# Performance work log

Measured on AMD Instinct MI355X. Metric: run time of the kernel, lower is better.

The kernel has to match this reference:

```python
import jax, jax.numpy as jnp
import numpy as np

B, N, E, D, F_IN, EDGE_DIM, VN = 128, 500, 1048576, 128, 5, 2, 10
NEG_FEAT = 0.01   # torch F.leaky_relu default
NEG_ATT = 0.2     # GAT attention slope


def _gat_layer(h_in, src, dst, edge_attr, W, b, a_src, a_dst, a_edge, We, n_nodes):
    # Edge-feature GAT conv: per-edge attention over (src, dst, edge) then
    # softmax-normalized scatter-aggregate onto destination nodes.
    h = h_in @ W                                  # [N, d]
    e = edge_attr @ We                            # [E, d] projected edge features
    logits = jax.nn.leaky_relu((h @ a_src)[src] + (h @ a_dst)[dst] + e @ a_edge,
                               negative_slope=NEG_ATT)    # [E]
    # segment softmax over incoming edges of each dst node
    m = jax.ops.segment_max(logits, dst, num_segments=n_nodes)
    ex = jnp.exp(logits - m[dst])
    denom = jax.ops.segment_sum(ex, dst, num_segments=n_nodes)
    alpha = ex / (denom[dst] + 1e-16)             # [E]
    msg = h[src] + e                              # [E, d]
    out = jax.ops.segment_sum(alpha[:, None] * msg, dst, num_segments=n_nodes)
    return out + b


def setup_inputs() -> dict:
    key = jax.random.key(0)
    ks = jax.random.split(key, 20)
    s = 0.05
    return {
        'x': jax.random.normal(ks[0], (B * N, F_IN), jnp.float32),
        'edge_index': jax.random.randint(ks[1], (2, E), 0, B * N, jnp.int64 if jax.config.jax_enable_x64 else jnp.int32).astype(jnp.int32),
        'edge_attr': jax.random.uniform(ks[2], (E, EDGE_DIM), jnp.float32),
        'curr_v_node_id': jax.random.randint(ks[3], (B,), 0, VN).astype(jnp.int32),
        'v_graph_embedding': jax.random.normal(ks[4], (B, D), jnp.float32),
        'v_node_dense_embeddings': jax.random.normal(ks[5], (B, VN, D), jnp.float32),
        'p_W': jax.random.normal(ks[6], (F_IN, D), jnp.float32) * s,
        'p_b': jnp.zeros((D,), jnp.float32),
        'Ws': jax.random.normal(ks[7], (4, D, D), jnp.float32) * s,
        'bs': jnp.zeros((4, D), jnp.float32),
        'a_srcs': jax.random.normal(ks[8], (4, D), jnp.float32) * s,
        'a_dsts': jax.random.normal(ks[9], (4, D), jnp.float32) * s,
        'a_edges': jax.random.normal(ks[10], (4, D), jnp.float32) * s,
        'Wes': jax.random.normal(ks[11], (4, EDGE_DIM, D), jnp.float32) * s,
        'W5': jax.random.normal(ks[12], (D, 1), jnp.float32) * s,
        'b5': jnp.zeros((1,), jnp.float32),
        'a_src5': jax.random.normal(ks[13], (1,), jnp.float32) * s,
        'a_dst5': jax.random.normal(ks[14], (1,), jnp.float32) * s,
        'a_edge5': jax.random.normal(ks[15], (1,), jnp.float32) * s,
        'We5': jax.random.normal(ks[16], (EDGE_DIM, 1), jnp.float32) * s,
    }


def reference(x, edge_index, edge_attr, curr_v_node_id, v_graph_embedding,
              v_node_dense_embeddings, p_W, p_b, Ws, bs, a_srcs, a_dsts,
              a_edges, Wes, W5, b5, a_src5, a_dst5, a_edge5, We5):
    n_nodes = x.shape[0]
    src, dst = edge_index[0], edge_index[1]
    # gather current v-node embedding: [B, D]
    curr_emb = v_node_dense_embeddings[jnp.arange(B), curr_v_node_id]
    # linear + leaky_relu then broadcast-add of graph/node context
    h = jax.nn.leaky_relu(x @ p_W + p_b, negative_slope=NEG_FEAT)  # [B*N, D]
    h = h.reshape(B, N, D) + v_graph_embedding[:, None, :] + curr_emb[:, None, :]
    h = h.reshape(B * N, D)
    # 4 hidden edge-feature GAT layers (128 -> 128) with leaky_relu
    for l in range(4):
        h = _gat_layer(h, src, dst, edge_attr, Ws[l], bs[l], a_srcs[l],
                       a_dsts[l], a_edges[l], Wes[l], n_nodes)
        h = jax.nn.leaky_relu(h, negative_slope=NEG_FEAT)
    # output layer (128 -> 1), no activation
    h = _gat_layer(h, src, dst, edge_attr, W5, b5, a_src5, a_dst5, a_edge5,
                   We5, n_nodes)                    # [B*N, 1]
    return h.reshape(B, N)
```

## Files before the change

kernel.cpp:

```cpp
#include <hip/hip_runtime.h>
#include <hip/hip_bf16.h>

#define BB   128
#define NN   500
#define NV   64000
#define EE   1048576
#define DD   128
#define FIN  5
#define VNN  10
#define NBUK 250
#define BCAP 8192

typedef unsigned int   uint32;
typedef unsigned short u16b;
typedef __attribute__((ext_vector_type(8))) short short8;
typedef __attribute__((ext_vector_type(4))) float float4v;

#define P_ASRC  0
#define P_ADST  512
#define P_WE    1024
#define P_BIAS  2048
#define P_W5    2560
#define P_CVEC  2688
#define P_SC5   2700
#define P_TOT   2816

static __device__ __forceinline__ float bf2f(__hip_bfloat16 v) { return __bfloat162float(v); }
static __device__ __forceinline__ float lo2f(uint32 u) { return __uint_as_float(u << 16); }
static __device__ __forceinline__ float hi2f(uint32 u) { return __uint_as_float(u & 0xFFFF0000u); }
static __device__ __forceinline__ uint32 f2bf_bits(float f) {
    uint32 u = __float_as_uint(f);
    return (u + 0x7FFFu + ((u >> 16) & 1u)) >> 16;
}
static __device__ __forceinline__ uint32 pack2(float a, float b) {
    return (f2bf_bits(a) & 0xFFFFu) | (f2bf_bits(b) << 16);
}
static __device__ __forceinline__ float ldf(const void* p, int i, int flag) {
    return flag ? ((const float*)p)[i] : bf2f(((const __hip_bfloat16*)p)[i]);
}

__global__ void sniff_kernel(const unsigned short* __restrict__ p16, int* __restrict__ FLAG) {
    __shared__ int sHigh, sZero;
    if (threadIdx.x == 0) { sHigh = 0; sZero = 0; }
    __syncthreads();
    unsigned short v = p16[2 * threadIdx.x];
    if (v >= 0x8000u) atomicOr(&sHigh, 1);
    if (v == 0)       atomicAdd(&sZero, 1);
    __syncthreads();
    if (threadIdx.x == 0) FLAG[0] = (sHigh || sZero >= 128) ? 1 : 0;
}

__global__ void zero_out_kernel(void* __restrict__ out, const int* __restrict__ FLAG, float tag) {
    int i = blockIdx.x * blockDim.x + threadIdx.x;
    if (i >= NV) return;
    float v = (i == 0) ? tag : 0.f;
    if (FLAG[0]) ((float*)out)[i] = v;
    else         ((u16b*)out)[i] = (u16b)f2bf_bits(v);
}

__global__ void prep_kernel(const void* __restrict__ Wes, const void* __restrict__ aeg,
                            const void* __restrict__ We5, const void* __restrict__ ae5,
                            const void* __restrict__ asr, const void* __restrict__ ads,
                            const void* __restrict__ bs, const void* __restrict__ W5,
                            const void* __restrict__ b5, const void* __restrict__ as5,
                            const void* __restrict__ ad5, const int* __restrict__ FLAG,
                            float* __restrict__ PAR) {
    const int flag = FLAG[0];
    if (blockIdx.x == 0) {
        for (int i = threadIdx.x; i < 512; i += 256) PAR[P_ASRC + i] = ldf(asr, i, flag);
    } else if (blockIdx.x == 1) {
        for (int i = threadIdx.x; i < 512; i += 256) PAR[P_ADST + i] = ldf(ads, i, flag);
    } else if (blockIdx.x == 2) {
        for (int i = threadIdx.x; i < 1024; i += 256) PAR[P_WE + i] = ldf(Wes, i, flag);
    } else if (blockIdx.x == 3) {
        for (int i = threadIdx.x; i < 512; i += 256) PAR[P_BIAS + i] = ldf(bs, i, flag);
    } else if (blockIdx.x == 4) {
        int tid = threadIdx.x;
        if (tid < 128) {
            PAR[P_W5 + tid] = ldf(W5, tid, flag);
        } else if (tid < 136) {
            int l = (tid - 128) >> 1, r = (tid - 128) & 1;
            float s = 0.f;
            for (int ch = 0; ch < DD; ++ch)
                s += ldf(Wes, l * 256 + r * DD + ch, flag) * ldf(aeg, l * DD + ch, flag);
            PAR[P_CVEC + l * 2 + r] = s;
        } else if (tid == 136) {
            float ae = ldf(ae5, 0, flag);
            float w0 = ldf(We5, 0, flag), w1 = ldf(We5, 1, flag);
            PAR[P_CVEC + 8] = w0 * ae; PAR[P_CVEC + 9] = w1 * ae;
            PAR[P_CVEC + 10] = w0;     PAR[P_CVEC + 11] = w1;
            PAR[P_SC5 + 0] = ldf(b5, 0, flag);
            PAR[P_SC5 + 1] = ldf(as5, 0, flag);
            PAR[P_SC5 + 2] = ldf(ad5, 0, flag);
        }
    }
}

__global__ __launch_bounds__(256) void prepack_kernel(const void* __restrict__ Ws,
                                                      const int* __restrict__ FLAG,
                                                      u16b* __restrict__ WB) {
    const int flag = FLAG[0];
    int t = blockIdx.x * 256 + threadIdx.x;
    int lane = t & 63;
    int frag = t >> 6;
    int nchunk = frag & 7, kblk = (frag >> 3) & 3, l = frag >> 5;
    int n = nchunk * 16 + (lane & 15);
    int kbase = kblk * 32 + (lane >> 4) * 8;
#pragma unroll
    for (int j = 0; j < 8; ++j) {
        int idx = l * 16384 + (kbase + j) * 128 + n;
        u16b bits = flag ? (u16b)f2bf_bits(((const float*)Ws)[idx])
                         : ((const u16b*)Ws)[idx];
        WB[(size_t)t * 8 + j] = bits;
    }
}

__global__ __launch_bounds__(256) void proj_kernel(
        const void* __restrict__ x, const void* __restrict__ pW,
        const void* __restrict__ pb, const int* __restrict__ curr,
        const void* __restrict__ vge, const void* __restrict__ vnd,
        const int* __restrict__ FLAG, uint32* __restrict__ H) {
    const int flag = FLAG[0];
    const int n = blockIdx.x * 4 + (threadIdx.x >> 6);
    const int lane = threadIdx.x & 63;
    const int b = n / NN;
    int cv = curr[b]; if ((unsigned)cv >= VNN) cv = 0;
    float xv[FIN];
#pragma unroll
    for (int k = 0; k < FIN; ++k) xv[k] = ldf(x, n * FIN + k, flag);
    const int ch = lane * 2;
    float s0 = ldf(pb, ch, flag), s1 = ldf(pb, ch + 1, flag);
#pragma unroll
    for (int k = 0; k < FIN; ++k) {
        s0 = fmaf(xv[k], ldf(pW, k * DD + ch, flag), s0);
        s1 = fmaf(xv[k], ldf(pW, k * DD + ch + 1, flag), s1);
    }
    s0 = (s0 > 0.f) ? s0 : 0.01f * s0;
    s1 = (s1 > 0.f) ? s1 : 0.01f * s1;
    s0 += ldf(vge, b * DD + ch, flag) + ldf(vnd, (b * VNN + cv) * DD + ch, flag);
    s1 += ldf(vge, b * DD + ch + 1, flag) + ldf(vnd, (b * VNN + cv) * DD + ch + 1, flag);
    H[(size_t)n * 64 + lane] = pack2(s0, s1);
}

__global__ void init_kernel(int* __restrict__ gcur, int* __restrict__ counts) {
    int t = blockIdx.x * 256 + threadIdx.x;
    if (t < NBUK) gcur[t] = t * BCAP;
    if (t < 512) counts[NV + t] = 0;
}

__global__ __launch_bounds__(256) void bucketize_kernel(
        const int* __restrict__ src, const int* __restrict__ dst,
        const void* __restrict__ eaP, const int* __restrict__ FLAG,
        int* __restrict__ gcur, uint32* __restrict__ bukx, uint32* __restrict__ buky) {
    __shared__ int cnt[256];
    __shared__ int cur[256];
    const int flag = FLAG[0];
    const int t = threadIdx.x;
    const int e0 = blockIdx.x * 4096;
    cnt[t] = 0;
    __syncthreads();
    int d[16];
#pragma unroll
    for (int i = 0; i < 16; ++i) {
        d[i] = dst[e0 + i * 256 + t];
        if ((unsigned)d[i] >= NV) d[i] = -1;
        if (d[i] >= 0) atomicAdd(&cnt[d[i] >> 8], 1);
    }
    __syncthreads();
    if (t < NBUK) {
        int c = cnt[t];
        cur[t] = c ? atomicAdd(&gcur[t], c) : 0;
    }
    __syncthreads();
#pragma unroll
    for (int i = 0; i < 16; ++i) {
        if (d[i] < 0) continue;
        int e = e0 + i * 256 + t;
        int b = d[i] >> 8;
        int s = src[e];
        if ((unsigned)s >= NV) s = 0;
        uint32 eb;
        if (flag) { float2 v = ((const float2*)eaP)[e]; eb = pack2(v.x, v.y); }
        else      eb = ((const uint32*)eaP)[e];
        int p = atomicAdd(&cur[b], 1);
        if (p < (b + 1) * BCAP) {
            bukx[p] = (uint32)((s & 0xFFFF) | ((d[i] & 255) << 16));
            buky[p] = eb;
        }
    }
}

__global__ __launch_bounds__(256) void bcount_kernel(
        const uint32* __restrict__ bukx, const int* __restrict__ gcur,
        int* __restrict__ counts) {
    __shared__ int c[256];
    const int b = blockIdx.x, t = threadIdx.x;
    c[t] = 0;
    __syncthreads();
    const int base = b * BCAP;
    int cnt = gcur[b] - base;
    if (cnt > BCAP) cnt = BCAP;
    for (int i = t; i < cnt; i += 256)
        atomicAdd(&c[(bukx[base + i] >> 16) & 255], 1);
    __syncthreads();
    counts[b * 256 + t] = c[t];
}

__global__ __launch_bounds__(256) void scan1_kernel(const int* __restrict__ counts,
                                                    int* __restrict__ row_ptr,
                                                    int* __restrict__ partials) {
    __shared__ int sdata[256];
    int tid = threadIdx.x;
    int4 v = ((const int4*)counts)[blockIdx.x * 256 + tid];
    int sum = v.x + v.y + v.z + v.w;
    sdata[tid] = sum;
    __syncthreads();
    int acc = sum;
    for (int off = 1; off < 256; off <<= 1) {
        int t = (tid >= off) ? sdata[tid - off] : 0;
        __syncthreads();
        acc += t;
        sdata[tid] = acc;
        __syncthreads();
    }
    int excl = acc - sum;
    int base = blockIdx.x * 1024 + tid * 4;
    int run = excl;
    if (base + 0 <= NV) row_ptr[base + 0] = run; run += v.x;
    if (base + 1 <= NV) row_ptr[base + 1] = run; run += v.y;
    if (base + 2 <= NV) row_ptr[base + 2] = run; run += v.z;
    if (base + 3 <= NV) row_ptr[base + 3] = run;
    if (tid == 255) partials[blockIdx.x] = acc;
}

__global__ __launch_bounds__(64) void scan2_kernel(const int* __restrict__ partials,
                                                   int* __restrict__ boff, int nb) {
    int lane = threadIdx.x;
    int v = (lane < nb) ? partials[lane] : 0;
    int orig = v;
#pragma unroll
    for (int off = 1; off < 64; off <<= 1) {
        int t = __shfl_up(v, off, 64);
        if (lane >= off) v += t;
    }
    boff[lane] = v - orig;
}

__global__ __launch_bounds__(256) void scan3_kernel(int* __restrict__ row_ptr,
                                                    const int* __restrict__ boff) {
    int add = boff[blockIdx.x];
    int base = blockIdx.x * 1024 + threadIdx.x * 4;
#pragma unroll
    for (int j = 0; j < 4; ++j) {
        int i = base + j;
        if (i <= NV) row_ptr[i] += add;
    }
}

__global__ __launch_bounds__(256) void bscatter_kernel(
        const uint32* __restrict__ bukx, const uint32* __restrict__ buky,
        const int* __restrict__ gcur, const int* __restrict__ row_ptr,
        int* __restrict__ csr_src, uint32* __restrict__ csr_ea) {
    __shared__ int cur[256];
    const int b = blockIdx.x, t = threadIdx.x;
    cur[t] = row_ptr[b * 256 + t];
    __syncthreads();
    const int base = b * BCAP;
    int cnt = gcur[b] - base;
    if (cnt > BCAP) cnt = BCAP;
    for (int i = t; i < cnt; i += 256) {
        uint32 x = bukx[base + i];
        uint32 y = buky[base + i];
        int p = atomicAdd(&cur[(x >> 16) & 255], 1);
        csr_src[p] = (int)(x & 0xFFFFu);
        csr_ea[p] = y;
    }
}

__global__ __launch_bounds__(256) void gemm_kernel(
        const uint32* __restrict__ Hu, const u16b* __restrict__ WBl,
        const float* __restrict__ PARl, uint32* __restrict__ HWu,
        float* __restrict__ ssrc, float* __restrict__ sdst) {
    __shared__ float hs[64 * 129];
    __shared__ float pp[512];
    const int tid = threadIdx.x;
    const int lane = tid & 63;
    const int wave = tid >> 6;
    const int quad = lane >> 4;
    const int n0 = blockIdx.x * 64;
    const int m = n0 + wave * 16 + (lane & 15);

    const u16b* hrow = (const u16b*)Hu + (size_t)m * 128;
    short8 a0 = *(const short8*)(hrow + 0  + quad * 8);
    short8 a1 = *(const short8*)(hrow + 32 + quad * 8);
    short8 a2 = *(const short8*)(hrow + 64 + quad * 8);
    short8 a3 = *(const short8*)(hrow + 96 + quad * 8);

#pragma unroll
    for (int nt = 0; nt < 8; ++nt) {
        const u16b* bbase = WBl + ((size_t)nt * 512 + lane * 8);
        short8 b0 = *(const short8*)(bbase + 0 * 4096);
        short8 b1 = *(const short8*)(bbase + 1 * 4096);
        short8 b2 = *(const short8*)(bbase + 2 * 4096);
        short8 b3 = *(const short8*)(bbase + 3 * 4096);
        float4v acc = {0.f, 0.f, 0.f, 0.f};
        acc = __builtin_amdgcn_mfma_f32_16x16x32_bf16(a0, b0, acc, 0, 0, 0);
        acc = __builtin_amdgcn_mfma_f32_16x16x32_bf16(a1, b1, acc, 0, 0, 0);
        acc = __builtin_amdgcn_mfma_f32_16x16x32_bf16(a2, b2, acc, 0, 0, 0);
        acc = __builtin_amdgcn_mfma_f32_16x16x32_bf16(a3, b3, acc, 0, 0, 0);
#pragma unroll
        for (int r = 0; r < 4; ++r)
            hs[(wave * 16 + quad * 4 + r) * 129 + nt * 16 + (lane & 15)] = acc[r];
    }
    __syncthreads();

    {
        const int mn = tid & 63, cg = tid >> 6;
        const float* Asr = PARl + P_ASRC;
        const float* Ads = PARl + P_ADST;
        const float* row = hs + mn * 129 + cg * 32;
        float ps = 0.f, pd = 0.f;
#pragma unroll
        for (int j = 0; j < 32; ++j) {
            float v = row[j];
            ps = fmaf(v, Asr[cg * 32 + j], ps);
            pd = fmaf(v, Ads[cg * 32 + j], pd);
        }
        pp[tid] = ps; pp[256 + tid] = pd;
    }
    __syncthreads();
    if (tid < 64) {
        ssrc[n0 + tid] = pp[tid] + pp[64 + tid] + pp[128 + tid] + pp[192 + tid];
        sdst[n0 + tid] = pp[256 + tid] + pp[320 + tid] + pp[384 + tid] + pp[448 + tid];
    }

#pragma unroll
    for (int i = 0; i < 4; ++i) {
        int flat = i * 2048 + tid * 8;
        int n = flat >> 7, c = flat & 127;
        const float* p = hs + n * 129 + c;
        uint4 v;
        v.x = pack2(p[0], p[1]); v.y = pack2(p[2], p[3]);
        v.z = pack2(p[4], p[5]); v.w = pack2(p[6], p[7]);
        *(uint4*)(HWu + (size_t)(n0 + n) * 64 + c / 2) = v;
    }
}

__global__ __launch_bounds__(256) void agg_kernel(
        const uint32* __restrict__ HWu, const float* __restrict__ ssrc,
        const float* __restrict__ sdst, const int* __restrict__ csr_src,
        const uint32* __restrict__ csr_ea, const int* __restrict__ row_ptr,
        const float* __restrict__ PAR, int layer, uint32* __restrict__ HoutU,
        float* __restrict__ hw5out, int wantw5) {
    const int lane = threadIdx.x & 63;
    const int n = blockIdx.x * 4 + (threadIdx.x >> 6);
    const int begin = __builtin_amdgcn_readfirstlane(row_ptr[n]);
    const int deg   = __builtin_amdgcn_readfirstlane(row_ptr[n + 1]) - begin;
    const float c0 = PAR[P_CVEC + 2 * layer], c1 = PAR[P_CVEC + 2 * layer + 1];
    const float sd = sdst[n];

    int   sv = 0;
    uint32 eb = 0;
    float L = -3.4e38f;
    if (lane < deg) {
        sv = csr_src[begin + lane];
        eb = csr_ea[begin + lane];
        L = fmaf(hi2f(eb), c1, fmaf(lo2f(eb), c0, ssrc[sv] + sd));
        L = (L > 0.f) ? L : 0.2f * L;
    }
    float m = L;
    for (int j0 = 64; j0 < deg; j0 += 64) {
        int j = j0 + lane;
        if (j < deg) {
            int s2 = csr_src[begin + j];
            uint32 e2 = csr_ea[begin + j];
            float L2 = fmaf(hi2f(e2), c1, fmaf(lo2f(e2), c0, ssrc[s2] + sd));
            L2 = (L2 > 0.f) ? L2 : 0.2f * L2;
            m = fmaxf(m, L2);
        }
    }
#pragma unroll
    for (int o = 32; o; o >>= 1) m = fmaxf(m, __shfl_xor(m, o, 64));

    float ex = (lane < deg) ? __expf(L - m) : 0.f;
    float dsum = ex, sx = ex * lo2f(eb), sy = ex * hi2f(eb);
    for (int j0 = 64; j0 < deg; j0 += 64) {
        int j = j0 + lane;
        if (j < deg) {
            int s2 = csr_src[begin + j];
            uint32 e2 = csr_ea[begin + j];
            float L2 = fmaf(hi2f(e2), c1, fmaf(lo2f(e2), c0, ssrc[s2] + sd));
            L2 = (L2 > 0.f) ? L2 : 0.2f * L2;
            float x2 = __expf(L2 - m);
            dsum += x2; sx = fmaf(x2, lo2f(e2), sx); sy = fmaf(x2, hi2f(e2), sy);
        }
    }
#pragma unroll
    for (int o = 32; o; o >>= 1) {
        dsum += __shfl_xor(dsum, o, 64);
        sx   += __shfl_xor(sx, o, 64);
        sy   += __shfl_xor(sy, o, 64);
    }

    const int dmain = (deg < 64) ? deg : 64;
    const uint32 exu = __float_as_uint(ex);
    float acc0 = 0.f, acc1 = 0.f;
    int jj = 0;
    for (; jj + 8 <= dmain; jj += 8) {
        int s8[8]; float e8[8]; uint32 hv[8];
#pragma unroll
        for (int q = 0; q < 8; ++q) {
            s8[q] = __builtin_amdgcn_readlane(sv, jj + q);
            e8[q] = __uint_as_float(__builtin_amdgcn_readlane((int)exu, jj + q));
        }
#pragma unroll
        for (int q = 0; q < 8; ++q) hv[q] = HWu[(size_t)s8[q] * 64 + lane];
#pragma unroll
        for (int q = 0; q < 8; ++q) {
            acc0 = fmaf(e8[q], lo2f(hv[q]), acc0);
            acc1 = fmaf(e8[q], hi2f(hv[q]), acc1);
        }
    }
    for (; jj < dmain; ++jj) {
        int s = __builtin_amdgcn_readlane(sv, jj);
        float e1v = __uint_as_float(__builtin_amdgcn_readlane((int)exu, jj));
        uint32 hb = HWu[(size_t)s * 64 + lane];
        acc0 = fmaf(e1v, lo2f(hb), acc0);
        acc1 = fmaf(e1v, hi2f(hb), acc1);
    }
    for (jj = 64; jj < deg; ++jj) {
        int s = csr_src[begin + jj];
        uint32 e2 = csr_ea[begin + jj];
        float L2 = fmaf(hi2f(e2), c1, fmaf(lo2f(e2), c0, ssrc[s] + sd));
        L2 = (L2 > 0.f) ? L2 : 0.2f * L2;
        float x2 = __expf(L2 - m);
        uint32 hb = HWu[(size_t)s * 64 + lane];
        acc0 = fmaf(x2, lo2f(hb), acc0);
        acc1 = fmaf(x2, hi2f(hb), acc1);
    }

    const int ch = lane * 2;
    const float* WEl = PAR + P_WE + layer * 256;
    const float inv = 1.f / (dsum + 1e-16f);
    const float* Bl = PAR + P_BIAS + layer * DD;
    float t0 = fmaf(sy, WEl[DD + ch],     fmaf(sx, WEl[ch],     acc0));
    float t1 = fmaf(sy, WEl[DD + ch + 1], fmaf(sx, WEl[ch + 1], acc1));
    float o0 = fmaf(t0, inv, Bl[ch]);
    float o1 = fmaf(t1, inv, Bl[ch + 1]);
    o0 = (o0 > 0.f) ? o0 : 0.01f * o0;
    o1 = (o1 > 0.f) ? o1 : 0.01f * o1;
    HoutU[(size_t)n * 64 + lane] = pack2(o0, o1);

    if (wantw5) {
        float p = o0 * PAR[P_W5 + ch] + o1 * PAR[P_W5 + ch + 1];
#pragma unroll
        for (int o = 32; o; o >>= 1) p += __shfl_xor(p, o, 64);
        if (lane == 0) hw5out[n] = p;
    }
}

__global__ __launch_bounds__(256) void final_kernel(
        const float* __restrict__ hw5, const int* __restrict__ csr_src,
        const uint32* __restrict__ csr_ea, const int* __restrict__ row_ptr,
        const float* __restrict__ PAR, const int* __restrict__ FLAG,
        void* __restrict__ out) {
    const int flag = FLAG[0];
    int lane = threadIdx.x & 63;
    int n = blockIdx.x * 4 + (threadIdx.x >> 6);
    int begin = __builtin_amdgcn_readfirstlane(row_ptr[n]);
    int deg   = __builtin_amdgcn_readfirstlane(row_ptr[n + 1]) - begin;
    float c50 = PAR[P_CVEC + 8], c51 = PAR[P_CVEC + 9];
    float ce0 = PAR[P_CVEC + 10], ce1 = PAR[P_CVEC + 11];
    float b5v = PAR[P_SC5], a5s = PAR[P_SC5 + 1];
    float hd = PAR[P_SC5 + 2] * hw5[n];

    float m = -3.4e38f;
    for (int j0 = 0; j0 < deg; j0 += 64) {
        int j = j0 + lane;
        if (j < deg) {
            int s = csr_src[begin + j];
            uint32 eb = csr_ea[begin + j];
            float L = fmaf(hi2f(eb), c51, fmaf(lo2f(eb), c50, fmaf(a5s, hw5[s], hd)));
            L = (L > 0.f) ? L : 0.2f * L;
            m = fmaxf(m, L);
        }
    }
#pragma unroll
    for (int o = 32; o; o >>= 1) m = fmaxf(m, __shfl_xor(m, o, 64));

    float dsum = 0.f, msum = 0.f;
    for (int j0 = 0; j0 < deg; j0 += 64) {
        int j = j0 + lane;
        if (j < deg) {
            int s = csr_src[begin + j];
            uint32 eb = csr_ea[begin + j];
            float hs5 = hw5[s];
            float L = fmaf(hi2f(eb), c51, fmaf(lo2f(eb), c50, fmaf(a5s, hs5, hd)));
            L = (L > 0.f) ? L : 0.2f * L;
            float ex = __expf(L - m);
            dsum += ex;
            msum = fmaf(ex, hs5 + fmaf(hi2f(eb), ce1, lo2f(eb) * ce0), msum);
        }
    }
#pragma unroll
    for (int o = 32; o; o >>= 1) {
        dsum += __shfl_xor(dsum, o, 64);
        msum += __shfl_xor(msum, o, 64);
    }
    if (lane == 0) {
        float r = msum / (dsum + 1e-16f) + b5v;
        if (flag) ((float*)out)[n] = r;
        else      ((u16b*)out)[n] = (u16b)f2bf_bits(r);
    }
}

extern "C" void kernel_launch(void* const* d_in, const int* in_sizes, int n_in,
                              void* d_out, int out_size, void* d_ws, size_t ws_size,
                              hipStream_t stream) {
    const void* x   = d_in[0];
    const int*  ei  = (const int*)d_in[1];
    const void* ea  = d_in[2];
    const int*  cur = (const int*)d_in[3];
    const void* vge = d_in[4];
    const void* vnd = d_in[5];
    const void* pW  = d_in[6];
    const void* pb  = d_in[7];
    const void* Ws  = d_in[8];
    const void* bs  = d_in[9];
    const void* asr = d_in[10];
    const void* ads = d_in[11];
    const void* aeg = d_in[12];
    const void* Wes = d_in[13];
    const void* W5  = d_in[14];
    const void* b5  = d_in[15];
    const void* as5 = d_in[16];
    const void* ad5 = d_in[17];
    const void* ae5 = d_in[18];
    const void* We5 = d_in[19];
    (void)in_sizes; (void)n_in; (void)out_size;

    const int* e_src = ei;
    const int* e_dst = ei + EE;

    size_t off = 0;
    char* base = (char*)d_ws;
    auto carve = [&](size_t bytes) {
        void* p = base + off;
        off += (bytes + 255) & ~(size_t)255;
        return p;
    };
    int*    FLAG   = (int*)carve(256);
    float*  PAR    = (float*)carve((size_t)P_TOT * 4);
    u16b*   WB     = (u16b*)carve(4 * DD * DD * 2);
    uint32* H0     = (uint32*)carve((size_t)NV * DD * 2);
    uint32* H1     = (uint32*)carve((size_t)NV * DD * 2);
    float*  SS     = (float*)carve(NV * 4);
    float*  SD     = (float*)carve(NV * 4);
    float*  HW5v   = (float*)carve(NV * 4);
    int*    COUNTS = (int*)carve(65536 * 4);
    int*    ROWPTR = (int*)carve(65536 * 4);
    int*    GCUR   = (int*)carve(256 * 4);
    int*    PART   = (int*)carve(256 * 4);
    int*    BOFF   = (int*)carve(256 * 4);
    int*    CSRS   = (int*)carve((size_t)EE * 4);
    uint32* CSREA  = (uint32*)carve((size_t)EE * 4);
    size_t need = off;

    uint32* BUKX = H1;
    uint32* BUKY = H1 + (size_t)NBUK * BCAP;

    sniff_kernel<<<1, 256, 0, stream>>>((const unsigned short*)ea, FLAG);

    if (need > ws_size) {
        zero_out_kernel<<<(NV + 255) / 256, 256, 0, stream>>>(
            d_out, FLAG, (float)(ws_size >> 20));
        return;
    }

    prep_kernel<<<5, 256, 0, stream>>>(Wes, aeg, We5, ae5, asr, ads, bs,
                                       W5, b5, as5, ad5, FLAG, PAR);
    prepack_kernel<<<32, 256, 0, stream>>>(Ws, FLAG, WB);
    proj_kernel<<<NV / 4, 256, 0, stream>>>(x, pW, pb, cur, vge, vnd, FLAG, H0);

    init_kernel<<<2, 256, 0, stream>>>(GCUR, COUNTS);
    bucketize_kernel<<<EE / 4096, 256, 0, stream>>>(e_src, e_dst, ea, FLAG,
                                                    GCUR, BUKX, BUKY);
    bcount_kernel<<<NBUK, 256, 0, stream>>>(BUKX, GCUR, COUNTS);
    scan1_kernel<<<63, 256, 0, stream>>>(COUNTS, ROWPTR, PART);
    scan2_kernel<<<1, 64, 0, stream>>>(PART, BOFF, 63);
    scan3_kernel<<<63, 256, 0, stream>>>(ROWPTR, BOFF);
    bscatter_kernel<<<NBUK, 256, 0, stream>>>(BUKX, BUKY, GCUR, ROWPTR,
                                              CSRS, CSREA);

    for (int l = 0; l < 4; ++l) {
        gemm_kernel<<<NV / 64, 256, 0, stream>>>(
            H0, WB + (size_t)l * 16384, PAR + l * DD, H1, SS, SD);
        agg_kernel<<<NV / 4, 256, 0, stream>>>(
            H1, SS, SD, CSRS, CSREA, ROWPTR, PAR, l, H0, HW5v, (l == 3) ? 1 : 0);
    }

    final_kernel<<<NV / 4, 256, 0, stream>>>(HW5v, CSRS, CSREA, ROWPTR, PAR,
                                             FLAG, d_out);
}
```

Before: 467.0 us.

## Prefetch neighbor feature rows before softmax in aggregation kernel

Issues the gathers of neighbour HW rows for the first 16 or 32 edges into registers before the max and softmax reductions, so that memory latency overlaps with the logit and exp computation. The weighted accumulation then reads the prefetched registers, and a scalar loop handles edges 32 to 63. Padded lanes use src index 0 with zero weight, so the extra loads are harmless. The 32 extra registers per thread may lower occupancy.

```diff
diff --git a/kernel.cpp b/kernel.cpp
--- a/kernel.cpp
+++ b/kernel.cpp
@@ -361,11 +361,32 @@
 
     int   sv = 0;
     uint32 eb = 0;
-    float L = -3.4e38f;
     if (lane < deg) {
         sv = csr_src[begin + lane];
         eb = csr_ea[begin + lane];
-        L = fmaf(hi2f(eb), c1, fmaf(lo2f(eb), c0, ssrc[sv] + sd));
+    }
+    const float ssv = ssrc[sv];
+
+    const int dmain = (deg < 64) ? deg : 64;
+    const int npad  = (dmain + 15) & ~15;
+
+    uint32 hA[16], hB[16];
+#pragma unroll
+    for (int q = 0; q < 16; ++q) {
+        int s = __builtin_amdgcn_readlane(sv, q);
+        hA[q] = HWu[(s << 6) + lane];
+    }
+    if (npad > 16) {
+#pragma unroll
+        for (int q = 0; q < 16; ++q) {
+            int s = __builtin_amdgcn_readlane(sv, 16 + q);
+            hB[q] = HWu[(s << 6) + lane];
+        }
+    }
+
+    float L = -3.4e38f;
+    if (lane < deg) {
+        L = fmaf(hi2f(eb), c1, fmaf(lo2f(eb), c0, ssv + sd));
         L = (L > 0.f) ? L : 0.2f * L;
     }
     float m = L;
@@ -402,33 +423,30 @@
         sy   += __shfl_xor(sy, o, 64);
     }
 
-    const int dmain = (deg < 64) ? deg : 64;
     const uint32 exu = __float_as_uint(ex);
     float acc0 = 0.f, acc1 = 0.f;
-    int jj = 0;
-    for (; jj + 8 <= dmain; jj += 8) {
-        int s8[8]; float e8[8]; uint32 hv[8];
-#pragma unroll
-        for (int q = 0; q < 8; ++q) {
-            s8[q] = __builtin_amdgcn_readlane(sv, jj + q);
-            e8[q] = __uint_as_float(__builtin_amdgcn_readlane((int)exu, jj + q));
-        }
-#pragma unroll
-        for (int q = 0; q < 8; ++q) hv[q] = HWu[(size_t)s8[q] * 64 + lane];
-#pragma unroll
-        for (int q = 0; q < 8; ++q) {
-            acc0 = fmaf(e8[q], lo2f(hv[q]), acc0);
-            acc1 = fmaf(e8[q], hi2f(hv[q]), acc1);
-        }
-    }
-    for (; jj < dmain; ++jj) {
-        int s = __builtin_amdgcn_readlane(sv, jj);
-        float e1v = __uint_as_float(__builtin_amdgcn_readlane((int)exu, jj));
-        uint32 hb = HWu[(size_t)s * 64 + lane];
-        acc0 = fmaf(e1v, lo2f(hb), acc0);
-        acc1 = fmaf(e1v, hi2f(hb), acc1);
-    }
-    for (jj = 64; jj < deg; ++jj) {
+#pragma unroll
+    for (int q = 0; q < 16; ++q) {
+        float w = __uint_as_float(__builtin_amdgcn_readlane((int)exu, q));
+        acc0 = fmaf(w, lo2f(hA[q]), acc0);
+        acc1 = fmaf(w, hi2f(hA[q]), acc1);
+    }
+    if (npad > 16) {
+#pragma unroll
+        for (int q = 0; q < 16; ++q) {
+            float w = __uint_as_float(__builtin_amdgcn_readlane((int)exu, 16 + q));
+            acc0 = fmaf(w, lo2f(hB[q]), acc0);
+            acc1 = fmaf(w, hi2f(hB[q]), acc1);
+        }
+    }
+    for (int j = 32; j < dmain; ++j) {
+        int s = __builtin_amdgcn_readlane(sv, j);
+        float w = __uint_as_float(__builtin_amdgcn_readlane((int)exu, j));
+        uint32 hb = HWu[(s << 6) + lane];
+        acc0 = fmaf(w, lo2f(hb), acc0);
+        acc1 = fmaf(w, hi2f(hb), acc1);
+    }
+    for (int jj = 64; jj < deg; ++jj) {
         int s = csr_src[begin + jj];
         uint32 e2 = csr_ea[begin + jj];
         float L2 = fmaf(hi2f(e2), c1, fmaf(lo2f(e2), c0, ssrc[s] + sd));
```

After: 441.9 us. 1.06x faster.
